# Optimization experiments

Measured on AMD Instinct MI355X. Metric: run time of the kernel, lower is better.

Reference implementation:

```python
import jax, jax.numpy as jnp
import numpy as np

IM_H, IM_W = 128, 128
HT_H, HT_W = 184, 180
N_VOTES = 1_500_000
B, C = 4, 32


def setup_inputs() -> dict:
    key = jax.random.key(0)
    k1, k2, k3, k4 = jax.random.split(key, 4)
    input_im = jax.random.normal(k1, (B, C, IM_H, IM_W), dtype=jnp.float32)
    im_idx = jax.random.randint(k2, (N_VOTES,), 0, IM_H * IM_W, dtype=jnp.int32)
    ht_idx = jax.random.randint(k3, (N_VOTES,), 0, HT_H * HT_W, dtype=jnp.int32)
    weight = jax.random.uniform(k4, (N_VOTES,), dtype=jnp.float32)
    return {"input_im": input_im, "im_idx": im_idx, "ht_idx": ht_idx, "weight": weight}


def reference(input_im, im_idx, ht_idx, weight):
    # input_im: [B, C, H, W] -> flatten pixels
    b, c, h, w = input_im.shape
    x = input_im.reshape(b, c, h * w)
    # gather voting pixel values and apply vote weights: [B, C, N]
    votes = x[:, :, im_idx] * weight  # broadcast weight over B, C
    # scatter-add into Hough bins (segment over leading axis)
    data = votes.transpose(2, 0, 1).reshape(votes.shape[2], b * c)  # [N, B*C]
    ht = jax.ops.segment_sum(data, ht_idx, num_segments=HT_H * HT_W)  # [HT, B*C]
    out = ht.T.reshape(b, c, HT_H, HT_W)
    return out
```

## Files before the change

kernel.cpp:

```cpp
#include <hip/hip_runtime.h>


#define HW   16384
#define BC   128
#define NHT  33120
#define RB   60
#define NB   552
#define CAPB 3712
#define CAPR 3528
#define CAPD 3712
#define VPB  4096
#define OFL_CAP 8192

typedef int iv4 __attribute__((ext_vector_type(4)));

__device__ __forceinline__ unsigned short f2bf(float f) {
  unsigned int u = __float_as_uint(f);
  u = (u + 0x7fff + ((u >> 16) & 1)) >> 16;
  return (unsigned short)u;
}

__global__ void k_init(const float* __restrict__ in, unsigned short* __restrict__ xTh,
                       int* __restrict__ gcur, int* __restrict__ ofl_cnt) {
  if (blockIdx.x == 2048) {
    int tid = threadIdx.y * 32 + threadIdx.x;
    for (int i = tid; i < NB; i += 256) gcur[i] = 0;
    if (tid == 0) *ofl_cnt = 0;
    return;
  }
  __shared__ float tile[32][33];
  int hw0 = (blockIdx.x & 511) * 32, bc0 = (blockIdx.x >> 9) * 32;
  int tx = threadIdx.x, ty = threadIdx.y;
#pragma unroll
  for (int k = 0; k < 32; k += 8)
    tile[ty + k][tx] = in[(size_t)(bc0 + ty + k) * HW + hw0 + tx];
  __syncthreads();
#pragma unroll
  for (int k = 0; k < 32; k += 8)
    xTh[(size_t)(hw0 + ty + k) * BC + bc0 + tx] = f2bf(tile[tx][ty + k]);
}

__global__ __launch_bounds__(1024) void k_bucket(
    const int* __restrict__ im, const int* __restrict__ ht,
    const float* __restrict__ wt, int n,
    int* __restrict__ gcur, int2* __restrict__ bkt,
    int* __restrict__ ofl_cnt, int2* __restrict__ ofl) {
  __shared__ int cnt[NB];
  __shared__ int base[NB];
  int tid = threadIdx.x;
  int i0 = blockIdx.x * VPB;
  for (int b = tid; b < NB; b += 1024) cnt[b] = 0;
  __syncthreads();
  int hv[4];
#pragma unroll
  for (int k = 0; k < 4; ++k) {
    int i = i0 + k * 1024 + tid;
    hv[k] = (i < n) ? ht[i] : -1;
    if (i < n) atomicAdd(&cnt[hv[k] / RB], 1);
  }
  __syncthreads();
  for (int b = tid; b < NB; b += 1024) {
    int c = cnt[b];
    base[b] = c ? atomicAdd(&gcur[b], c) : 0;
    cnt[b] = 0;
  }
  __syncthreads();
#pragma unroll
  for (int k = 0; k < 4; ++k) {
    int i = i0 + k * 1024 + tid;
    if (i < n) {
      int h = hv[k];
      int b = h / RB;
      int hl = h - b * RB;
      int pos = base[b] + atomicAdd(&cnt[b], 1);
      if (pos < CAPR) {
        bkt[(size_t)b * CAPB + pos] =
            make_int2((im[i] & 0x3FFF) | (hl << 14), __float_as_int(wt[i]));
      } else {
        int o = atomicAdd(ofl_cnt, 1);
        if (o < OFL_CAP)
          ofl[o] = make_int2((im[i] & 0x3FFF) | (h << 14), __float_as_int(wt[i]));
      }
    }
  }
}

__global__ __launch_bounds__(1024) void k_accum8(
    const int2* __restrict__ bkt, const int* __restrict__ gcur,
    const unsigned short* __restrict__ xTh, float* __restrict__ out,
    const int* __restrict__ ofl_cnt, const int2* __restrict__ ofl) {
  __shared__ int2 sdst[CAPD];
  __shared__ float lacc[RB * 129];
  __shared__ int hist[RB], off[RB], pcnt[RB], cur[RB];
  int2* buf = (int2*)lacc;
  int tid = threadIdx.x;
  int r = blockIdx.x;
  int ht0 = r * RB;
  int n = gcur[r];
  if (n > CAPR) n = CAPR;
  const int2* s = bkt + (size_t)r * CAPB;
  for (int i = tid; i < n; i += 1024) buf[i] = s[i];
  if (tid < RB) hist[tid] = 0;
  __syncthreads();
  for (int i = tid; i < n; i += 1024)
    atomicAdd(&hist[buf[i].x >> 14], 1);
  __syncthreads();
  if (tid < 64) {
    int v = (tid < RB) ? ((hist[tid] + 3) & ~3) : 0;
    int inc = v;
#pragma unroll
    for (int d = 1; d < 64; d <<= 1) {
      int t = __shfl_up(inc, d);
      if (tid >= d) inc += t;
    }
    if (tid < RB) { off[tid] = inc - v; pcnt[tid] = v; cur[tid] = 0; }
  }
  __syncthreads();
  if (tid < RB) {
    for (int d = hist[tid]; d < pcnt[tid]; ++d)
      sdst[off[tid] + d] = make_int2(0, 0);
  }
  for (int i = tid; i < n; i += 1024) {
    int2 v = buf[i];
    int hl = v.x >> 14;
    int pos = off[hl] + atomicAdd(&cur[hl], 1);
    sdst[pos] = make_int2(v.x & 0x3FFF, v.y);
  }
  __syncthreads();

  int w = __builtin_amdgcn_readfirstlane(tid >> 6);
  int lane = tid & 63;
  int q = lane >> 4;
  int cg = lane & 15;
  const unsigned short* xb = xTh + (cg << 3);
  if (w < 15) {
#pragma unroll
    for (int bi = 0; bi < 4; ++bi) {
      int bin = w * 4 + bi;
      int o = off[bin], nb = pcnt[bin];
      float acc[8] = {0, 0, 0, 0, 0, 0, 0, 0};

#define GATHER_FMA(IM, W)                                                     \
  {                                                                           \
    iv4 xd = *(const iv4*)(xb + ((size_t)(IM) << 7));                         \
    _Pragma("unroll") for (int c = 0; c < 4; ++c) {                           \
      float lo = __uint_as_float(((unsigned int)xd[c]) << 16);                \
      float hi = __uint_as_float(((unsigned int)xd[c]) & 0xffff0000u);        \
      acc[2 * c]     = fmaf((W), lo, acc[2 * c]);                             \
      acc[2 * c + 1] = fmaf((W), hi, acc[2 * c + 1]);                         \
    }                                                                         \
  }

      int i = 0;
      for (; i + 8 <= nb; i += 8) {
        int2 r0 = sdst[o + i + q];
        int2 r1 = sdst[o + i + 4 + q];
        GATHER_FMA(r0.x, __int_as_float(r0.y));
        GATHER_FMA(r1.x, __int_as_float(r1.y));
      }
      for (; i < nb; i += 4) {
        int2 r0 = sdst[o + i + q];
        GATHER_FMA(r0.x, __int_as_float(r0.y));
      }
#undef GATHER_FMA

#pragma unroll
      for (int k = 0; k < 8; ++k) {
        float t = acc[k] + __shfl_xor(acc[k], 16);
        acc[k] = t + __shfl_xor(t, 32);
      }
      if (lane < 16) {
        int row = bin * 129 + (cg << 3);
#pragma unroll
        for (int k = 0; k < 8; ++k) lacc[row + k] = acc[k];
      }
    }
  }
  __syncthreads();

  int cnt = *ofl_cnt;
  if (cnt > 0) {
    if (cnt > OFL_CAP) cnt = OFL_CAP;
    if (tid < 128) {
      for (int v = 0; v < cnt; ++v) {
        int2 rec = ofl[v];
        int h = rec.x >> 14;
        if (h >= ht0 && h < ht0 + RB) {
          int imv = rec.x & 0x3FFF;
          float wv = __int_as_float(rec.y);
          float xv = __uint_as_float(((unsigned int)xTh[((size_t)imv << 7) + tid]) << 16);
          lacc[(h - ht0) * 129 + tid] += wv * xv;
        }
      }
    }
    __syncthreads();
  }

  int ch = tid >> 3;
  for (int jj = tid & 7; jj < RB; jj += 8)
    out[(size_t)ch * NHT + ht0 + jj] = lacc[jj * 129 + ch];
}

extern "C" void kernel_launch(void* const* d_in, const int* in_sizes, int n_in,
                              void* d_out, int out_size, void* d_ws, size_t ws_size,
                              hipStream_t stream) {
  const float* input_im = (const float*)d_in[0];
  const int*   im_idx   = (const int*)d_in[1];
  const int*   ht_idx   = (const int*)d_in[2];
  const float* weight   = (const float*)d_in[3];
  float*       out      = (float*)d_out;
  const int N = in_sizes[1];

  char* w = (char*)d_ws;
  unsigned short* xTh = (unsigned short*)(w + 0);
  int2*  bkt     = (int2*) (w + 4194304);
  int*   gcur    = (int*)  (w + 20586496);
  int*   ofl_cnt = (int*)  (w + 20588800);
  int2*  ofl     = (int2*) (w + 20588928);

  k_init<<<2049, dim3(32, 8), 0, stream>>>(input_im, xTh, gcur, ofl_cnt);
  k_bucket<<<(N + VPB - 1) / VPB, 1024, 0, stream>>>(im_idx, ht_idx, weight, N,
                                                     gcur, bkt, ofl_cnt, ofl);
  k_accum8<<<NB, 1024, 0, stream>>>(bkt, gcur, xTh, out, ofl_cnt, ofl);
}
```

Baseline: 138.3 us.

## Fuse transpose and bucketing kernels into one launch, spread bins across all waves

The bf16 transpose of the input image and the vote bucketing now run as two roles inside a single 1024-thread launch, so they overlap instead of running as separate kernels. The counter and overflow reset becomes a hipMemsetAsync, with ofl_cnt moved so it sits inside the cleared range. The accumulate kernel now hands bins to all 16 waves in round-robin instead of 15 waves taking four bins each. Trade-offs: a memset call is added, and each transpose block now covers four tiles with 1024 threads.

```diff
diff --git a/kernel.cpp b/kernel.cpp
--- a/kernel.cpp
+++ b/kernel.cpp
@@ -10,6 +10,8 @@
 #define CAPR 3528
 #define CAPD 3712
 #define VPB  4096
+#define NBK  367
+#define NTR  512
 #define OFL_CAP 8192
 
 typedef int iv4 __attribute__((ext_vector_type(4)));
@@ -20,34 +22,35 @@
   return (unsigned short)u;
 }
 
-__global__ void k_init(const float* __restrict__ in, unsigned short* __restrict__ xTh,
-                       int* __restrict__ gcur, int* __restrict__ ofl_cnt) {
-  if (blockIdx.x == 2048) {
-    int tid = threadIdx.y * 32 + threadIdx.x;
-    for (int i = tid; i < NB; i += 256) gcur[i] = 0;
-    if (tid == 0) *ofl_cnt = 0;
-    return;
-  }
-  __shared__ float tile[32][33];
-  int hw0 = (blockIdx.x & 511) * 32, bc0 = (blockIdx.x >> 9) * 32;
-  int tx = threadIdx.x, ty = threadIdx.y;
-#pragma unroll
-  for (int k = 0; k < 32; k += 8)
-    tile[ty + k][tx] = in[(size_t)(bc0 + ty + k) * HW + hw0 + tx];
-  __syncthreads();
-#pragma unroll
-  for (int k = 0; k < 32; k += 8)
-    xTh[(size_t)(hw0 + ty + k) * BC + bc0 + tx] = f2bf(tile[tx][ty + k]);
-}
-
-__global__ __launch_bounds__(1024) void k_bucket(
+__global__ __launch_bounds__(1024) void k_work(
+    const float* __restrict__ in, unsigned short* __restrict__ xTh,
     const int* __restrict__ im, const int* __restrict__ ht,
     const float* __restrict__ wt, int n,
     int* __restrict__ gcur, int2* __restrict__ bkt,
     int* __restrict__ ofl_cnt, int2* __restrict__ ofl) {
-  __shared__ int cnt[NB];
-  __shared__ int base[NB];
+  __shared__ __align__(16) char smem[4 * 32 * 33 * 4];
   int tid = threadIdx.x;
+
+  if (blockIdx.x >= NBK) {
+    float* tilef = (float*)smem;
+    int sub = tid >> 8;
+    int t256 = tid & 255;
+    int tx = t256 & 31, ty = t256 >> 5;
+    int tileIdx = (blockIdx.x - NBK) * 4 + sub;
+    int hw0 = (tileIdx & 511) * 32, bc0 = (tileIdx >> 9) * 32;
+    float* tile = tilef + sub * (32 * 33);
+#pragma unroll
+    for (int k = 0; k < 32; k += 8)
+      tile[(ty + k) * 33 + tx] = in[(size_t)(bc0 + ty + k) * HW + hw0 + tx];
+    __syncthreads();
+#pragma unroll
+    for (int k = 0; k < 32; k += 8)
+      xTh[(size_t)(hw0 + ty + k) * BC + bc0 + tx] = f2bf(tile[tx * 33 + ty + k]);
+    return;
+  }
+
+  int* cnt = (int*)smem;
+  int* base = cnt + NB;
   int i0 = blockIdx.x * VPB;
   for (int b = tid; b < NB; b += 1024) cnt[b] = 0;
   __syncthreads();
@@ -133,12 +136,9 @@
   int q = lane >> 4;
   int cg = lane & 15;
   const unsigned short* xb = xTh + (cg << 3);
-  if (w < 15) {
-#pragma unroll
-    for (int bi = 0; bi < 4; ++bi) {
-      int bin = w * 4 + bi;
-      int o = off[bin], nb = pcnt[bin];
-      float acc[8] = {0, 0, 0, 0, 0, 0, 0, 0};
+  for (int bin = w; bin < RB; bin += 16) {
+    int o = off[bin], nb = pcnt[bin];
+    float acc[8] = {0, 0, 0, 0, 0, 0, 0, 0};
 
 #define GATHER_FMA(IM, W)                                                     \
   {                                                                           \
@@ -151,29 +151,28 @@
     }                                                                         \
   }
 
-      int i = 0;
-      for (; i + 8 <= nb; i += 8) {
-        int2 r0 = sdst[o + i + q];
-        int2 r1 = sdst[o + i + 4 + q];
-        GATHER_FMA(r0.x, __int_as_float(r0.y));
-        GATHER_FMA(r1.x, __int_as_float(r1.y));
-      }
-      for (; i < nb; i += 4) {
-        int2 r0 = sdst[o + i + q];
-        GATHER_FMA(r0.x, __int_as_float(r0.y));
-      }
+    int i = 0;
+    for (; i + 8 <= nb; i += 8) {
+      int2 r0 = sdst[o + i + q];
+      int2 r1 = sdst[o + i + 4 + q];
+      GATHER_FMA(r0.x, __int_as_float(r0.y));
+      GATHER_FMA(r1.x, __int_as_float(r1.y));
+    }
+    for (; i < nb; i += 4) {
+      int2 r0 = sdst[o + i + q];
+      GATHER_FMA(r0.x, __int_as_float(r0.y));
+    }
 #undef GATHER_FMA
 
 #pragma unroll
-      for (int k = 0; k < 8; ++k) {
-        float t = acc[k] + __shfl_xor(acc[k], 16);
-        acc[k] = t + __shfl_xor(t, 32);
-      }
-      if (lane < 16) {
-        int row = bin * 129 + (cg << 3);
-#pragma unroll
-        for (int k = 0; k < 8; ++k) lacc[row + k] = acc[k];
-      }
+    for (int k = 0; k < 8; ++k) {
+      float t = acc[k] + __shfl_xor(acc[k], 16);
+      acc[k] = t + __shfl_xor(t, 32);
+    }
+    if (lane < 16) {
+      int row = bin * 129 + (cg << 3);
+#pragma unroll
+      for (int k = 0; k < 8; ++k) lacc[row + k] = acc[k];
     }
   }
   __syncthreads();
@@ -215,11 +214,11 @@
   unsigned short* xTh = (unsigned short*)(w + 0);
   int2*  bkt     = (int2*) (w + 4194304);
   int*   gcur    = (int*)  (w + 20586496);
-  int*   ofl_cnt = (int*)  (w + 20588800);
-  int2*  ofl     = (int2*) (w + 20588928);
-
-  k_init<<<2049, dim3(32, 8), 0, stream>>>(input_im, xTh, gcur, ofl_cnt);
-  k_bucket<<<(N + VPB - 1) / VPB, 1024, 0, stream>>>(im_idx, ht_idx, weight, N,
-                                                     gcur, bkt, ofl_cnt, ofl);
+  int*   ofl_cnt = (int*)  (w + 20588704);
+  int2*  ofl     = (int2*) (w + 20589056);
+
+  hipMemsetAsync(gcur, 0, 2212, stream);
+  k_work<<<NBK + NTR, 1024, 0, stream>>>(input_im, xTh, im_idx, ht_idx, weight, N,
+                                         gcur, bkt, ofl_cnt, ofl);
   k_accum8<<<NB, 1024, 0, stream>>>(bkt, gcur, xTh, out, ofl_cnt, ofl);
 }
```

Measured after the change: 139.0 us. Within noise of the previous version (+0.5%).
